# Kernel optimization log

Measured on AMD Instinct MI355X. Metric: run time of the kernel, lower is better.

Reference implementation:

```python
import jax, jax.numpy as jnp
import numpy as np

T, B, D = 200, 1024, 128
T_OBS = 140
L = 20       # rec_dims: encoder latent per mean/std
LAT = 32     # latents: generative latent dim
GRU_U = 200  # gru_units
UNITS = 100  # hidden units of ODE-func / z0 nets


def _lin(key, fan_in, fan_out):
    return jax.random.normal(key, (fan_in, fan_out), jnp.float32) / jnp.sqrt(jnp.float32(fan_in))


def setup_inputs() -> dict:
    key = jax.random.key(0)
    ks = jax.random.split(key, 20)
    gin = 2 * L + 2 * D  # GRU input: (mean,std) + (data,mask)
    inp = {
        "truth": jax.random.normal(ks[0], (T, B, D), jnp.float32),
        "t": jnp.arange(T, dtype=jnp.float32),
        "obs_idx": jnp.sort(jax.random.randint(ks[1], (T_OBS,), 0, T)),
        "eps": jax.random.normal(ks[2], (B, LAT), jnp.float32),
        # encoder ODE func (rec_layers=1 hidden layer of UNITS)
        "enc_w1": _lin(ks[3], L, UNITS), "enc_b1": jnp.zeros(UNITS, jnp.float32),
        "enc_w2": _lin(ks[4], UNITS, L), "enc_b2": jnp.zeros(L, jnp.float32),
        # GRU unit: update / reset / new-state nets
        "gru_uw1": _lin(ks[5], gin, GRU_U), "gru_ub1": jnp.zeros(GRU_U, jnp.float32),
        "gru_uw2": _lin(ks[6], GRU_U, 2 * L), "gru_ub2": jnp.zeros(2 * L, jnp.float32),
        "gru_rw1": _lin(ks[7], gin, GRU_U), "gru_rb1": jnp.zeros(GRU_U, jnp.float32),
        "gru_rw2": _lin(ks[8], GRU_U, 2 * L), "gru_rb2": jnp.zeros(2 * L, jnp.float32),
        "gru_nw1": _lin(ks[9], gin, GRU_U), "gru_nb1": jnp.zeros(GRU_U, jnp.float32),
        "gru_nw2": _lin(ks[10], GRU_U, 2 * L), "gru_nb2": jnp.zeros(2 * L, jnp.float32),
        # transform hidden -> z0 (mean,std)
        "z0_w1": _lin(ks[11], 2 * L, UNITS), "z0_b1": jnp.zeros(UNITS, jnp.float32),
        "z0_w2": _lin(ks[12], UNITS, 2 * LAT), "z0_b2": jnp.zeros(2 * LAT, jnp.float32),
        # decoder ODE func (gen_layers=2 hidden layers of UNITS)
        "dec_w1": _lin(ks[13], LAT, UNITS), "dec_b1": jnp.zeros(UNITS, jnp.float32),
        "dec_w2": _lin(ks[14], UNITS, UNITS), "dec_b2": jnp.zeros(UNITS, jnp.float32),
        "dec_w3": _lin(ks[15], UNITS, LAT), "dec_b3": jnp.zeros(LAT, jnp.float32),
        # readout latent -> data space
        "out_w": _lin(ks[16], LAT, D), "out_b": jnp.zeros(D, jnp.float32),
    }
    return inp


def _rk4(f, y, dt):
    k1 = f(y)
    k2 = f(y + 0.5 * dt * k1)
    k3 = f(y + 0.5 * dt * k2)
    k4 = f(y + dt * k3)
    return y + (dt / 6.0) * (k1 + 2.0 * k2 + 2.0 * k3 + k4)


def reference(truth, t, obs_idx, eps,
              enc_w1, enc_b1, enc_w2, enc_b2,
              gru_uw1, gru_ub1, gru_uw2, gru_ub2,
              gru_rw1, gru_rb1, gru_rw2, gru_rb2,
              gru_nw1, gru_nb1, gru_nw2, gru_nb2,
              z0_w1, z0_b1, z0_w2, z0_b2,
              dec_w1, dec_b1, dec_w2, dec_b2, dec_w3, dec_b3,
              out_w, out_b):
    enc_f = lambda y: jnp.tanh(y @ enc_w1 + enc_b1) @ enc_w2 + enc_b2
    dec_f = lambda z: (jnp.tanh(jnp.tanh(z @ dec_w1 + dec_b1) @ dec_w2 + dec_b2)
                       @ dec_w3 + dec_b3)

    # ----- ODE-RNN encoder, run_backwards=True over observed timesteps -----
    x_obs = truth[obs_idx][::-1]                     # [To, B, D], time-reversed
    t_obs = t[obs_idx][::-1]
    dts = jnp.concatenate([jnp.zeros(1, t.dtype), jnp.diff(t_obs)])  # <=0 steps

    def enc_step(carry, inp):
        ym, ys = carry                               # [B,L] each
        x, dt = inp
        ym = _rk4(enc_f, ym, dt)                     # evolve mean between obs
        xm = jnp.concatenate([x, jnp.ones_like(x)], -1)   # data + mask(=1)
        y = jnp.concatenate([ym, ys], -1)            # [B, 2L]
        yc = jnp.concatenate([y, xm], -1)            # [B, 2L+2D]
        u = jax.nn.sigmoid(jnp.tanh(yc @ gru_uw1 + gru_ub1) @ gru_uw2 + gru_ub2)
        r = jax.nn.sigmoid(jnp.tanh(yc @ gru_rw1 + gru_rb1) @ gru_rw2 + gru_rb2)
        nc = jnp.concatenate([y * r, xm], -1)
        ns = jnp.tanh(nc @ gru_nw1 + gru_nb1) @ gru_nw2 + gru_nb2
        nm, nsd = ns[:, :L], jnp.abs(ns[:, L:])
        new_y = (1.0 - u) * jnp.concatenate([nm, nsd], -1) + u * y
        return (new_y[:, :L], new_y[:, L:]), None

    nb = truth.shape[1]
    init = (jnp.zeros((nb, L), truth.dtype), jnp.zeros((nb, L), truth.dtype))
    (ym, ys), _ = jax.lax.scan(enc_step, init, (x_obs, dts))

    # ----- z0 posterior and sample (n_traj_samples=1) -----
    h = jnp.tanh(jnp.concatenate([ym, ys], -1) @ z0_w1 + z0_b1) @ z0_w2 + z0_b2
    z0_mean, z0_std = h[:, :LAT], jnp.abs(h[:, LAT:])
    z = z0_mean + eps * z0_std                       # [B, LAT]

    # ----- Neural ODE decoder over time_steps_to_predict = t -----
    def dec_step(zc, dt):
        zn = _rk4(dec_f, zc, dt)
        return zn, zn
    _, zs = jax.lax.scan(dec_step, z, jnp.diff(t))
    sol = jnp.concatenate([z[None], zs], 0)          # [T, B, LAT]

    out = sol @ out_w + out_b                        # [T, B, D]
    return jnp.transpose(out, (1, 0, 2))[None]       # [1, B, T, D]
```

## Files before the change

### kernel.cpp

```cpp
#include <hip/hip_runtime.h>
#include <math.h>

#define BB 1024
#define DD 128
#define NWG 256
#define CH 28
#define NCH 5

#define WS_WPACK 0
#define WS_B1E   81920
#define WS_W1Y   82560
#define WS_Y     106560
#define WS_Z     147520
#define WS_HPRE  180288
#define WS_SOL   180288

__device__ __forceinline__ float tanh_fast(float x) {
    const float t = __builtin_amdgcn_exp2f(x * 2.88539008177793f);
    return 1.f - 2.f * __builtin_amdgcn_rcpf(t + 1.f);
}

__global__ __launch_bounds__(256) void prep_kernel(
    const float* __restrict__ uw1, const float* __restrict__ ub1,
    const float* __restrict__ rw1, const float* __restrict__ rb1,
    const float* __restrict__ nw1, const float* __restrict__ nb1,
    float* __restrict__ ws)
{
    int tid = blockIdx.x * blockDim.x + threadIdx.x;
    int nth = gridDim.x * blockDim.x;
    for (int idx = tid; idx < 128 * 640; idx += nth) {
        int k = idx / 640, j = idx - k * 640;
        float v = 0.f;
        if (j < 600) {
            int g = j / 200, jj = j - g * 200;
            const float* w1 = (g == 0) ? uw1 : (g == 1) ? rw1 : nw1;
            v = w1[(40 + k) * 200 + jj];
        }
        ws[WS_WPACK + idx] = v;
    }
    for (int j = tid; j < 640; j += nth) {
        float s = 0.f;
        if (j < 600) {
            int g = j / 200, jj = j - g * 200;
            const float* w1 = (g == 0) ? uw1 : (g == 1) ? rw1 : nw1;
            const float* b1 = (g == 0) ? ub1 : (g == 1) ? rb1 : nb1;
            s = b1[jj];
            for (int k = 168; k < 296; ++k) s += w1[k * 200 + jj];
        }
        ws[WS_B1E + j] = s;
    }
    for (int idx = tid; idx < 40 * 600; idx += nth) {
        int k = idx / 600, j = idx - k * 600;
        int g = j / 200, jj = j - g * 200;
        const float* w1 = (g == 0) ? uw1 : (g == 1) ? rw1 : nw1;
        ws[WS_W1Y + idx] = w1[k * 200 + jj];
    }
}

__global__ __launch_bounds__(256) void hpre_gemm(
    const float* __restrict__ truth, const int* __restrict__ obs_idx,
    const float* __restrict__ ws, float* __restrict__ hpre, int s0)
{
    __shared__ float sx[64][68];
    __shared__ float sw[64][132];
    const int t0 = threadIdx.x;
    const int jt = blockIdx.x % 5;
    const int bt = (blockIdx.x / 5) % 16;
    const int sl = blockIdx.x / 80;
    const int oi = obs_idx[139 - (s0 + sl)];
    const int b0 = bt * 64;
    const float* wpack = ws + WS_WPACK;
    const float* b1e   = ws + WS_B1E;

    const int jj  = t0 & 15;
    const int bb4 = t0 >> 4;
    float acc[8][4];
#pragma unroll
    for (int m = 0; m < 8; ++m)
#pragma unroll
        for (int q = 0; q < 4; ++q) acc[m][q] = 0.f;

    for (int kh = 0; kh < 2; ++kh) {
        __syncthreads();
        for (int i = t0; i < 64 * 16; i += 256) {
            int bb = i >> 4, kq = i & 15;
            const float4 v = *(const float4*)&truth[((size_t)oi * BB + b0 + bb) * DD + kh * 64 + kq * 4];
            *(float4*)&sx[bb][kq * 4] = v;
        }
        for (int i = t0; i < 64 * 32; i += 256) {
            int kk = i >> 5, jq = i & 31;
            const float4 v = *(const float4*)&wpack[(kh * 64 + kk) * 640 + jt * 128 + jq * 4];
            *(float4*)&sw[kk][jq * 4] = v;
        }
        __syncthreads();
#pragma unroll 4
        for (int k = 0; k < 64; ++k) {
            float xv[4], wv[8];
#pragma unroll
            for (int q = 0; q < 4; ++q) xv[q] = sx[bb4 * 4 + q][k];
#pragma unroll
            for (int m = 0; m < 8; ++m) wv[m] = sw[k][jj + 16 * m];
#pragma unroll
            for (int m = 0; m < 8; ++m)
#pragma unroll
                for (int q = 0; q < 4; ++q) acc[m][q] += wv[m] * xv[q];
        }
    }
    const int bblk = bt * 16 + bb4;
#pragma unroll
    for (int m = 0; m < 8; ++m) {
        int j = jt * 128 + jj + 16 * m;
        if (j < 600) {
            float be = b1e[j];
#pragma unroll
            for (int q = 0; q < 4; ++q)
                hpre[(size_t)((sl * 256 + bblk) * 4 + q) * 600 + j] = acc[m][q] + be;
        }
    }
}

__global__ __launch_bounds__(256, 1) void enc_chunk(
    const float* __restrict__ tg, const int* __restrict__ obs_idx,
    const float* __restrict__ eps,
    const float* __restrict__ ew1, const float* __restrict__ eb1,
    const float* __restrict__ ew2, const float* __restrict__ eb2,
    const float* __restrict__ uw2, const float* __restrict__ ub2,
    const float* __restrict__ rw2, const float* __restrict__ rb2,
    const float* __restrict__ nw2, const float* __restrict__ nb2,
    const float* __restrict__ z0w1, const float* __restrict__ z0b1,
    const float* __restrict__ z0w2, const float* __restrict__ z0b2,
    float* __restrict__ ws, int s0)
{
    __shared__ float s_t[200];
    __shared__ int   s_oi[140];
    __shared__ __align__(16) float s_y[40][4];
    __shared__ __align__(16) float s_ytmp[20][4];
    __shared__ float s_kacc[20][4];
    __shared__ __align__(16) float s_hid[4][104];
    __shared__ float s_pe[20][4][2];
    __shared__ __align__(16) float s_ew1t[100 * 20];
    __shared__ __align__(16) float s_w2n[40 * 212];
    __shared__ __align__(16) float s_hur[4][416];
    __shared__ __align__(16) float s_hn[4][208];
    __shared__ float s_pw[80][4][4];
    __shared__ float s_pn[40][4][4];
    __shared__ float s_u[40][4];
    __shared__ __align__(16) float s_yr[40][4];
    __shared__ float s_z0o[4][64];

    const int t0 = threadIdx.x;
    const int bblk = blockIdx.x;
    const int b0 = bblk * 4;
    const float* hpre = ws + WS_HPRE;

    float rgy[3][40];
    float rew2h[52];
    float rw2q[2][52];
    float eb1_r = 0.f, eb2_r = 0.f, bur_r = 0.f, bn_r = 0.f;

    if (t0 < 200) {
#pragma unroll
        for (int g = 0; g < 3; ++g)
#pragma unroll
            for (int k = 0; k < 40; ++k)
                rgy[g][k] = ws[WS_W1Y + k * 600 + g * 200 + t0];
    }
    if (t0 < 100) eb1_r = eb1[t0];
    if (t0 < 160) {
        const int c2 = t0 % 20, kh = t0 / 80;
#pragma unroll
        for (int i = 0; i < 52; ++i) {
            const int row = kh * 52 + i;
            rew2h[i] = (row < 100) ? ew2[row * 20 + c2] : 0.f;
        }
    }
    if (t0 < 80) eb2_r = eb2[t0 % 20];
    if (t0 < 160) {
        const int p = t0 % 20, g = (t0 / 20) % 2, kq = t0 / 40;
        const float* w2 = g ? rw2 : uw2;
#pragma unroll
        for (int j = 0; j < 2; ++j)
#pragma unroll
            for (int i = 0; i < 52; ++i) {
                const int row = kq * 52 + i;
                rw2q[j][i] = (row < 200) ? w2[row * 40 + p + 20 * j] : 0.f;
            }
        bur_r = ((t0 % 80) < 40) ? ub2[t0 % 80] : rb2[(t0 % 80) - 40];
        bn_r = nb2[t0 % 40];
    }

    for (int i = t0; i < 2000; i += 256) { int k = i / 100, c = i % 100; s_ew1t[c * 20 + k] = ew1[i]; }
    for (int i = t0; i < 40 * 212; i += 256) { int o = i / 212, k = i % 212; s_w2n[i] = (k < 200) ? nw2[k * 40 + o] : 0.f; }
    for (int i = t0; i < 200; i += 256) s_t[i] = tg[i];
    for (int i = t0; i < 140; i += 256) s_oi[i] = obs_idx[i];
    if (t0 < 160) { int k = t0 % 40, b = t0 / 40; s_y[k][b] = s0 ? ws[WS_Y + k * 1024 + b0 + b] : 0.f; }
    if (t0 < 4) {
#pragma unroll
        for (int i = 0; i < 4; ++i) s_hid[t0][100 + i] = 0.f;
#pragma unroll
        for (int i = 0; i < 8; ++i) { s_hur[t0][200 + i] = 0.f; s_hur[t0][408 + i] = 0.f; s_hn[t0][200 + i] = 0.f; }
    }
    __syncthreads();

    for (int sl = 0; sl < CH; ++sl) {
        const int s = s0 + sl;
        const int oi = s_oi[139 - s];
        const float dt = (s == 0) ? 0.f : (s_t[oi] - s_t[s_oi[140 - s]]);

        float hpu[4], hpr[4], hpn[4];
        if (t0 < 200) {
#pragma unroll
            for (int q = 0; q < 4; ++q) {
                const size_t r = (size_t)((sl * 256 + bblk) * 4 + q) * 600;
                hpu[q] = hpre[r + t0];
                hpr[q] = hpre[r + 200 + t0];
                hpn[q] = hpre[r + 400 + t0];
            }
        }

#pragma unroll 1
        for (int e = 0; e < 4; ++e) {
            if (t0 < 100) {
                const int c = t0;
                float a[4] = {eb1_r, eb1_r, eb1_r, eb1_r};
#pragma unroll
                for (int i = 0; i < 5; ++i) {
                    const float4 wv = *(const float4*)&s_ew1t[c * 20 + 4 * i];
                    const float wk[4] = {wv.x, wv.y, wv.z, wv.w};
#pragma unroll
                    for (int kk = 0; kk < 4; ++kk) {
                        const int k = 4 * i + kk;
                        const float4 yv = (e == 0) ? *(const float4*)&s_y[k][0]
                                                   : *(const float4*)&s_ytmp[k][0];
                        a[0] += wk[kk] * yv.x; a[1] += wk[kk] * yv.y;
                        a[2] += wk[kk] * yv.z; a[3] += wk[kk] * yv.w;
                    }
                }
#pragma unroll
                for (int b = 0; b < 4; ++b) s_hid[b][c] = tanhf(a[b]);
            }
            __syncthreads();
            if (t0 < 160) {
                const int c2 = t0 % 20, b = (t0 / 20) % 4, kh = t0 / 80;
                float acc = 0.f;
#pragma unroll
                for (int i = 0; i < 13; ++i) {
                    const float4 hv = *(const float4*)&s_hid[b][kh * 52 + 4 * i];
                    acc += hv.x * rew2h[4 * i] + hv.y * rew2h[4 * i + 1]
                         + hv.z * rew2h[4 * i + 2] + hv.w * rew2h[4 * i + 3];
                }
                s_pe[c2][b][kh] = acc;
            }
            __syncthreads();
            if (t0 < 80) {
                const int c2 = t0 % 20, b = t0 / 20;
                const float kv = eb2_r + s_pe[c2][b][0] + s_pe[c2][b][1];
                const float y0 = s_y[c2][b];
                if (e == 0)      { s_kacc[c2][b] = kv;        s_ytmp[c2][b] = y0 + 0.5f * dt * kv; }
                else if (e == 1) { s_kacc[c2][b] += 2.f * kv; s_ytmp[c2][b] = y0 + 0.5f * dt * kv; }
                else if (e == 2) { s_kacc[c2][b] += 2.f * kv; s_ytmp[c2][b] = y0 + dt * kv; }
                else             { s_y[c2][b] = y0 + (dt / 6.f) * (s_kacc[c2][b] + kv); }
            }
            __syncthreads();
        }

        if (t0 < 200) {
            float au[4], ar[4];
#pragma unroll
            for (int b = 0; b < 4; ++b) { au[b] = hpu[b]; ar[b] = hpr[b]; }
#pragma unroll
            for (int k = 0; k < 40; ++k) {
                const float4 yv = *(const float4*)&s_y[k][0];
                const float wu = rgy[0][k], wr = rgy[1][k];
                au[0] += wu * yv.x; au[1] += wu * yv.y; au[2] += wu * yv.z; au[3] += wu * yv.w;
                ar[0] += wr * yv.x; ar[1] += wr * yv.y; ar[2] += wr * yv.z; ar[3] += wr * yv.w;
            }
#pragma unroll
            for (int b = 0; b < 4; ++b) {
                s_hur[b][t0] = tanhf(au[b]);
                s_hur[b][208 + t0] = tanhf(ar[b]);
            }
        }
        __syncthreads();

        if (t0 < 160) {
            const int p = t0 % 20, g = (t0 / 20) % 2, kq = t0 / 40;
            const int goff = g * 208;
            float a1[4] = {0.f, 0.f, 0.f, 0.f}, a2[4] = {0.f, 0.f, 0.f, 0.f};
#pragma unroll
            for (int i = 0; i < 13; ++i) {
                const float wa = rw2q[0][4 * i], wb = rw2q[0][4 * i + 1],
                            wc = rw2q[0][4 * i + 2], wd = rw2q[0][4 * i + 3];
                const float we = rw2q[1][4 * i], wf = rw2q[1][4 * i + 1],
                            wg = rw2q[1][4 * i + 2], wh = rw2q[1][4 * i + 3];
#pragma unroll
                for (int b = 0; b < 4; ++b) {
                    const float4 hv = *(const float4*)&s_hur[b][goff + kq * 52 + 4 * i];
                    a1[b] += hv.x * wa + hv.y * wb + hv.z * wc + hv.w * wd;
                    a2[b] += hv.x * we + hv.y * wf + hv.z * wg + hv.w * wh;
                }
            }
            const int o1 = 40 * g + p, o2 = o1 + 20;
#pragma unroll
            for (int b = 0; b < 4; ++b) { s_pw[o1][b][kq] = a1[b]; s_pw[o2][b][kq] = a2[b]; }
        }
        __syncthreads();

        if (t0 < 160) {
            const int o = t0 % 80, bp = t0 / 80;
#pragma unroll
            for (int j = 0; j < 2; ++j) {
                const int b = 2 * bp + j;
                const float v = bur_r + s_pw[o][b][0] + s_pw[o][b][1] + s_pw[o][b][2] + s_pw[o][b][3];
                const float sg = 1.f / (1.f + expf(-v));
                if (o < 40) s_u[o][b] = sg;
                else        s_yr[o - 40][b] = s_y[o - 40][b] * sg;
            }
        }
        __syncthreads();

        if (t0 < 200) {
            float an[4];
#pragma unroll
            for (int b = 0; b < 4; ++b) an[b] = hpn[b];
#pragma unroll
            for (int k = 0; k < 40; ++k) {
                const float4 yv = *(const float4*)&s_yr[k][0];
                const float w = rgy[2][k];
                an[0] += w * yv.x; an[1] += w * yv.y; an[2] += w * yv.z; an[3] += w * yv.w;
            }
#pragma unroll
            for (int b = 0; b < 4; ++b) s_hn[b][t0] = tanhf(an[b]);
        }
        __syncthreads();

        if (t0 < 160) {
            const int o = t0 % 40, kq = t0 / 40;
            float an[4] = {0.f, 0.f, 0.f, 0.f};
#pragma unroll
            for (int i = 0; i < 13; ++i) {
                const float4 wv = *(const float4*)&s_w2n[o * 212 + kq * 52 + 4 * i];
#pragma unroll
                for (int b = 0; b < 4; ++b) {
                    const float4 hv = *(const float4*)&s_hn[b][kq * 52 + 4 * i];
                    an[b] += hv.x * wv.x + hv.y * wv.y + hv.z * wv.z + hv.w * wv.w;
                }
            }
#pragma unroll
            for (int b = 0; b < 4; ++b) s_pn[o][b][kq] = an[b];
        }
        __syncthreads();

        if (t0 < 160) {
            const int o = t0 % 40, b = t0 / 40;
            const float v = bn_r + s_pn[o][b][0] + s_pn[o][b][1] + s_pn[o][b][2] + s_pn[o][b][3];
            const float cand = (o < 20) ? v : fabsf(v);
            const float uu = s_u[o][b];
            s_y[o][b] = (1.f - uu) * cand + uu * s_y[o][b];
        }
        __syncthreads();
    }

    if (s0 + CH == 140) {
        if (t0 < 100) {
            const int c = t0;
            float a[4] = {z0b1[c], z0b1[c], z0b1[c], z0b1[c]};
#pragma unroll
            for (int k = 0; k < 40; ++k) {
                const float4 yv = *(const float4*)&s_y[k][0];
                const float w = z0w1[k * 100 + c];
                a[0] += w * yv.x; a[1] += w * yv.y; a[2] += w * yv.z; a[3] += w * yv.w;
            }
#pragma unroll
            for (int b = 0; b < 4; ++b) s_hid[b][c] = tanhf(a[b]);
        }
        __syncthreads();
        {
            const int b = t0 / 64, u = t0 % 64;
            float acc = z0b2[u];
#pragma unroll
            for (int i = 0; i < 25; ++i) {
                const float4 hv = *(const float4*)&s_hid[b][4 * i];
                acc += hv.x * z0w2[(4 * i) * 64 + u] + hv.y * z0w2[(4 * i + 1) * 64 + u]
                     + hv.z * z0w2[(4 * i + 2) * 64 + u] + hv.w * z0w2[(4 * i + 3) * 64 + u];
            }
            s_z0o[b][u] = acc;
        }
        __syncthreads();
        if (t0 < 128) {
            const int b = t0 / 32, i = t0 % 32;
            const int gb = b0 + b;
            ws[WS_Z + gb * 32 + i] = s_z0o[b][i] + eps[gb * 32 + i] * fabsf(s_z0o[b][32 + i]);
        }
    }
    if (t0 < 160) {
        const int k = t0 % 40, b = t0 / 40;
        ws[WS_Y + k * 1024 + b0 + b] = s_y[k][b];
    }
}

__global__ __launch_bounds__(256, 3) void dec_kernel(
    const float* __restrict__ tg,
    const float* __restrict__ dw1, const float* __restrict__ db1,
    const float* __restrict__ dw2, const float* __restrict__ db2,
    const float* __restrict__ dw3, const float* __restrict__ db3,
    float* __restrict__ ws)
{
    __shared__ float s_t[200];
    __shared__ __align__(16) float s_z[32];
    __shared__ __align__(16) float s_h1[112];
    __shared__ __align__(16) float s_h2[112];
    __shared__ float s_p1[4][100];
    __shared__ float s_p2[4][100];
    __shared__ float s_p3[8][32];

    const int t0 = threadIdx.x;
    const int w  = t0 >> 6;
    const int l  = t0 & 63;
    const int hk = l >> 5;
    const int batch = blockIdx.x;

    const int c0 = l;
    const int c1 = 64 + l;
    const bool has1 = (l < 36);
    const int j3 = l & 31;

    float rw1a[8], rw1b[8], rw2a[28], rw2b[28], rw3[14];
#pragma unroll
    for (int i = 0; i < 8; ++i) {
        rw1a[i] = dw1[(8 * w + i) * 100 + c0];
        rw1b[i] = has1 ? dw1[(8 * w + i) * 100 + c1] : 0.f;
    }
#pragma unroll
    for (int i = 0; i < 28; ++i) {
        const int row = 28 * w + i;
        const bool v = (row < 100);
        rw2a[i] = v ? dw2[row * 100 + c0] : 0.f;
        rw2b[i] = (v && has1) ? dw2[row * 100 + c1] : 0.f;
    }
#pragma unroll
    for (int i = 0; i < 14; ++i) {
        const int row = 28 * w + 14 * hk + i;
        rw3[i] = (row < 100) ? dw3[row * 32 + j3] : 0.f;
    }
    float b1_r = 0.f, b2_r = 0.f, b3_r = 0.f;
    if (t0 < 100) { b1_r = db1[t0]; b2_r = db2[t0]; }
    if (t0 < 32)  b3_r = db3[t0];

    for (int i = t0; i < 200; i += 256) s_t[i] = tg[i];
    if (t0 >= 100 && t0 < 112) { s_h1[t0] = 0.f; s_h2[t0] = 0.f; }

    float z_r = 0.f, ka_r = 0.f;
    if (t0 < 32) { z_r = ws[WS_Z + (size_t)batch * 32 + t0]; s_z[t0] = z_r; }
    __syncthreads();

    for (int s = 0; s < 200; ++s) {
        if (t0 < 32)
            ws[WS_SOL + (size_t)(s * 1024 + batch) * 32 + t0] = z_r;
        if (s == 199) break;
        const float dtv = s_t[s + 1] - s_t[s];

#pragma unroll 1
        for (int e = 0; e < 4; ++e) {
            {
                const float4 za = *(const float4*)&s_z[8 * w];
                const float4 zb = *(const float4*)&s_z[8 * w + 4];
                float a0 = za.x * rw1a[0] + za.y * rw1a[1] + za.z * rw1a[2] + za.w * rw1a[3]
                         + zb.x * rw1a[4] + zb.y * rw1a[5] + zb.z * rw1a[6] + zb.w * rw1a[7];
                float a1 = za.x * rw1b[0] + za.y * rw1b[1] + za.z * rw1b[2] + za.w * rw1b[3]
                         + zb.x * rw1b[4] + zb.y * rw1b[5] + zb.z * rw1b[6] + zb.w * rw1b[7];
                s_p1[w][c0] = a0;
                if (has1) s_p1[w][c1] = a1;
            }
            __syncthreads();
            if (t0 < 100)
                s_h1[t0] = tanh_fast(b1_r + s_p1[0][t0] + s_p1[1][t0] + s_p1[2][t0] + s_p1[3][t0]);
            __syncthreads();

            {
                float a2 = 0.f, a3 = 0.f;
#pragma unroll
                for (int i = 0; i < 7; ++i) {
                    const float4 hv = *(const float4*)&s_h1[28 * w + 4 * i];
                    a2 += hv.x * rw2a[4 * i] + hv.y * rw2a[4 * i + 1]
                        + hv.z * rw2a[4 * i + 2] + hv.w * rw2a[4 * i + 3];
                    a3 += hv.x * rw2b[4 * i] + hv.y * rw2b[4 * i + 1]
                        + hv.z * rw2b[4 * i + 2] + hv.w * rw2b[4 * i + 3];
                }
                s_p2[w][c0] = a2;
                if (has1) s_p2[w][c1] = a3;
            }
            __syncthreads();
            if (t0 < 100)
                s_h2[t0] = tanh_fast(b2_r + s_p2[0][t0] + s_p2[1][t0] + s_p2[2][t0] + s_p2[3][t0]);
            __syncthreads();

            {
                float ap = 0.f;
#pragma unroll
                for (int i = 0; i < 7; ++i) {
                    const float2 hv = *(const float2*)&s_h2[28 * w + 14 * hk + 2 * i];
                    ap += hv.x * rw3[2 * i] + hv.y * rw3[2 * i + 1];
                }
                s_p3[2 * w + hk][j3] = ap;
            }
            __syncthreads();
            if (t0 < 32) {
                const float kj = b3_r
                    + s_p3[0][t0] + s_p3[1][t0] + s_p3[2][t0] + s_p3[3][t0]
                    + s_p3[4][t0] + s_p3[5][t0] + s_p3[6][t0] + s_p3[7][t0];
                float zs;
                if (e == 0)      { ka_r = kj;        zs = z_r + 0.5f * dtv * kj; }
                else if (e == 1) { ka_r += 2.f * kj; zs = z_r + 0.5f * dtv * kj; }
                else if (e == 2) { ka_r += 2.f * kj; zs = z_r + dtv * kj; }
                else             { z_r += (dtv / 6.f) * (ka_r + kj); zs = z_r; }
                s_z[t0] = zs;
            }
            __syncthreads();
        }
    }
}

__global__ __launch_bounds__(256) void proj_kernel(
    const float* __restrict__ ow, const float* __restrict__ ob,
    const float* __restrict__ ws, float* __restrict__ out)
{
    const int t0 = threadIdx.x;
    const int d = t0 & 127, half = t0 >> 7;
    float rw[32];
#pragma unroll
    for (int k = 0; k < 32; ++k) rw[k] = ow[k * 128 + d];
    const float bo = ob[d];
    const int sb0 = blockIdx.x * 64 + half * 32;
#pragma unroll 2
    for (int m = 0; m < 32; ++m) {
        const int sb = sb0 + m;
        const int s = sb >> 10, b = sb & 1023;
        const float4* zp = (const float4*)&ws[WS_SOL + (size_t)sb * 32];
        float acc = bo;
#pragma unroll
        for (int kq = 0; kq < 8; ++kq) {
            const float4 zv = zp[kq];
            acc += zv.x * rw[4 * kq] + zv.y * rw[4 * kq + 1]
                 + zv.z * rw[4 * kq + 2] + zv.w * rw[4 * kq + 3];
        }
        out[((size_t)b * 200 + s) * 128 + d] = acc;
    }
}

extern "C" void kernel_launch(void* const* d_in, const int* in_sizes, int n_in,
                              void* d_out, int out_size, void* d_ws, size_t ws_size,
                              hipStream_t stream)
{
    const float* truth = (const float*)d_in[0];
    const float* tg    = (const float*)d_in[1];
    const int*   oi    = (const int*)d_in[2];
    const float* eps   = (const float*)d_in[3];
    const float* ew1   = (const float*)d_in[4];
    const float* eb1   = (const float*)d_in[5];
    const float* ew2   = (const float*)d_in[6];
    const float* eb2   = (const float*)d_in[7];
    const float* uw1   = (const float*)d_in[8];
    const float* ub1   = (const float*)d_in[9];
    const float* uw2   = (const float*)d_in[10];
    const float* ub2   = (const float*)d_in[11];
    const float* rw1   = (const float*)d_in[12];
    const float* rb1   = (const float*)d_in[13];
    const float* rw2   = (const float*)d_in[14];
    const float* rb2   = (const float*)d_in[15];
    const float* nw1   = (const float*)d_in[16];
    const float* nb1   = (const float*)d_in[17];
    const float* nw2   = (const float*)d_in[18];
    const float* nb2   = (const float*)d_in[19];
    const float* z0w1  = (const float*)d_in[20];
    const float* z0b1  = (const float*)d_in[21];
    const float* z0w2  = (const float*)d_in[22];
    const float* z0b2  = (const float*)d_in[23];
    const float* dw1   = (const float*)d_in[24];
    const float* db1   = (const float*)d_in[25];
    const float* dw2   = (const float*)d_in[26];
    const float* db2   = (const float*)d_in[27];
    const float* dw3   = (const float*)d_in[28];
    const float* db3   = (const float*)d_in[29];
    const float* ow    = (const float*)d_in[30];
    const float* ob    = (const float*)d_in[31];
    float* ws  = (float*)d_ws;
    float* out = (float*)d_out;

    prep_kernel<<<dim3(120), dim3(256), 0, stream>>>(uw1, ub1, rw1, rb1, nw1, nb1, ws);
    for (int c = 0; c < NCH; ++c) {
        hpre_gemm<<<dim3(CH * 16 * 5), dim3(256), 0, stream>>>(truth, oi, ws, ws + WS_HPRE, c * CH);
        enc_chunk<<<dim3(NWG), dim3(256), 0, stream>>>(
            tg, oi, eps, ew1, eb1, ew2, eb2, uw2, ub2, rw2, rb2, nw2, nb2,
            z0w1, z0b1, z0w2, z0b2, ws, c * CH);
    }
    dec_kernel<<<dim3(1024), dim3(256), 0, stream>>>(tg, dw1, db1, dw2, db2, dw3, db3, ws);
    proj_kernel<<<dim3(3200), dim3(256), 0, stream>>>(ow, ob, ws, out);
}
```

Before: 4.514 ms.

## Cut decoder RK4 barriers by having each wave reduce its own hidden rows

The decoder ODE loop is re-partitioned so each wave owns a contiguous slice of hidden rows (24 or 28). That wave reduces the partial sums for its rows, applies tanh and consumes only those rows in the next layer. Every wave also redundantly computes the final k and z update for all 32 latents. Together these remove three of the six block-wide barriers per RK4 function evaluation, which matters in this latency-bound single-batch-per-block loop. In exchange the partial-sum buffers are padded and the last-layer matmul does more per-wave work with redundant reductions. Correctness now relies on intra-wave LDS ordering and on the benign race of waves writing identical s_z values.

```diff
diff --git a/kernel.cpp b/kernel.cpp
--- a/kernel.cpp
+++ b/kernel.cpp
@@ -408,24 +408,25 @@
 {
     __shared__ float s_t[200];
     __shared__ __align__(16) float s_z[32];
-    __shared__ __align__(16) float s_h1[112];
-    __shared__ __align__(16) float s_h2[112];
-    __shared__ float s_p1[4][100];
-    __shared__ float s_p2[4][100];
-    __shared__ float s_p3[8][32];
+    __shared__ __align__(16) float s_h1[100];
+    __shared__ __align__(16) float s_h2[100];
+    __shared__ float s_p1[4][128];
+    __shared__ float s_p2[4][128];
+    __shared__ float s_p3[4][32];
 
     const int t0 = threadIdx.x;
     const int w  = t0 >> 6;
     const int l  = t0 & 63;
-    const int hk = l >> 5;
     const int batch = blockIdx.x;
 
     const int c0 = l;
     const int c1 = 64 + l;
     const bool has1 = (l < 36);
     const int j3 = l & 31;
-
-    float rw1a[8], rw1b[8], rw2a[28], rw2b[28], rw3[14];
+    const int r0 = 24 * w;
+    const int n2 = (w == 3) ? 28 : 24;
+
+    float rw1a[8], rw1b[8], rw2a[28], rw2b[28], rw3[28];
 #pragma unroll
     for (int i = 0; i < 8; ++i) {
         rw1a[i] = dw1[(8 * w + i) * 100 + c0];
@@ -433,25 +434,21 @@
     }
 #pragma unroll
     for (int i = 0; i < 28; ++i) {
-        const int row = 28 * w + i;
-        const bool v = (row < 100);
+        const int row = r0 + i;
+        const bool v = (i < n2);
         rw2a[i] = v ? dw2[row * 100 + c0] : 0.f;
         rw2b[i] = (v && has1) ? dw2[row * 100 + c1] : 0.f;
-    }
-#pragma unroll
-    for (int i = 0; i < 14; ++i) {
-        const int row = 28 * w + 14 * hk + i;
-        rw3[i] = (row < 100) ? dw3[row * 32 + j3] : 0.f;
-    }
-    float b1_r = 0.f, b2_r = 0.f, b3_r = 0.f;
-    if (t0 < 100) { b1_r = db1[t0]; b2_r = db2[t0]; }
-    if (t0 < 32)  b3_r = db3[t0];
+        rw3[i]  = v ? dw3[row * 32 + j3] : 0.f;
+    }
+    float b1c = 0.f, b2c = 0.f;
+    if (l < n2) { b1c = db1[r0 + l]; b2c = db2[r0 + l]; }
+    const float b3c = db3[j3];
 
     for (int i = t0; i < 200; i += 256) s_t[i] = tg[i];
-    if (t0 >= 100 && t0 < 112) { s_h1[t0] = 0.f; s_h2[t0] = 0.f; }
-
-    float z_r = 0.f, ka_r = 0.f;
-    if (t0 < 32) { z_r = ws[WS_Z + (size_t)batch * 32 + t0]; s_z[t0] = z_r; }
+
+    float z_r = ws[WS_Z + (size_t)batch * 32 + j3];
+    float ka_r = 0.f;
+    if (l < 32) s_z[l] = z_r;
     __syncthreads();
 
     for (int s = 0; s < 200; ++s) {
@@ -470,53 +467,76 @@
                 float a1 = za.x * rw1b[0] + za.y * rw1b[1] + za.z * rw1b[2] + za.w * rw1b[3]
                          + zb.x * rw1b[4] + zb.y * rw1b[5] + zb.z * rw1b[6] + zb.w * rw1b[7];
                 s_p1[w][c0] = a0;
-                if (has1) s_p1[w][c1] = a1;
+                s_p1[w][c1] = a1;
             }
             __syncthreads();
-            if (t0 < 100)
-                s_h1[t0] = tanh_fast(b1_r + s_p1[0][t0] + s_p1[1][t0] + s_p1[2][t0] + s_p1[3][t0]);
-            __syncthreads();
+
+            if (l < n2) {
+                const int r = r0 + l;
+                s_h1[r] = tanh_fast(b1c + s_p1[0][r] + s_p1[1][r] + s_p1[2][r] + s_p1[3][r]);
+            }
 
             {
                 float a2 = 0.f, a3 = 0.f;
-#pragma unroll
-                for (int i = 0; i < 7; ++i) {
-                    const float4 hv = *(const float4*)&s_h1[28 * w + 4 * i];
-                    a2 += hv.x * rw2a[4 * i] + hv.y * rw2a[4 * i + 1]
-                        + hv.z * rw2a[4 * i + 2] + hv.w * rw2a[4 * i + 3];
-                    a3 += hv.x * rw2b[4 * i] + hv.y * rw2b[4 * i + 1]
-                        + hv.z * rw2b[4 * i + 2] + hv.w * rw2b[4 * i + 3];
+                if (w == 3) {
+#pragma unroll
+                    for (int i = 0; i < 7; ++i) {
+                        const float4 hv = *(const float4*)&s_h1[72 + 4 * i];
+                        a2 += hv.x * rw2a[4 * i] + hv.y * rw2a[4 * i + 1]
+                            + hv.z * rw2a[4 * i + 2] + hv.w * rw2a[4 * i + 3];
+                        a3 += hv.x * rw2b[4 * i] + hv.y * rw2b[4 * i + 1]
+                            + hv.z * rw2b[4 * i + 2] + hv.w * rw2b[4 * i + 3];
+                    }
+                } else {
+#pragma unroll
+                    for (int i = 0; i < 6; ++i) {
+                        const float4 hv = *(const float4*)&s_h1[r0 + 4 * i];
+                        a2 += hv.x * rw2a[4 * i] + hv.y * rw2a[4 * i + 1]
+                            + hv.z * rw2a[4 * i + 2] + hv.w * rw2a[4 * i + 3];
+                        a3 += hv.x * rw2b[4 * i] + hv.y * rw2b[4 * i + 1]
+                            + hv.z * rw2b[4 * i + 2] + hv.w * rw2b[4 * i + 3];
+                    }
                 }
                 s_p2[w][c0] = a2;
-                if (has1) s_p2[w][c1] = a3;
+                s_p2[w][c1] = a3;
             }
             __syncthreads();
-            if (t0 < 100)
-                s_h2[t0] = tanh_fast(b2_r + s_p2[0][t0] + s_p2[1][t0] + s_p2[2][t0] + s_p2[3][t0]);
-            __syncthreads();
+
+            if (l < n2) {
+                const int r = r0 + l;
+                s_h2[r] = tanh_fast(b2c + s_p2[0][r] + s_p2[1][r] + s_p2[2][r] + s_p2[3][r]);
+            }
 
             {
                 float ap = 0.f;
-#pragma unroll
-                for (int i = 0; i < 7; ++i) {
-                    const float2 hv = *(const float2*)&s_h2[28 * w + 14 * hk + 2 * i];
-                    ap += hv.x * rw3[2 * i] + hv.y * rw3[2 * i + 1];
+                if (w == 3) {
+#pragma unroll
+                    for (int i = 0; i < 7; ++i) {
+                        const float4 hv = *(const float4*)&s_h2[72 + 4 * i];
+                        ap += hv.x * rw3[4 * i] + hv.y * rw3[4 * i + 1]
+                            + hv.z * rw3[4 * i + 2] + hv.w * rw3[4 * i + 3];
+                    }
+                } else {
+#pragma unroll
+                    for (int i = 0; i < 6; ++i) {
+                        const float4 hv = *(const float4*)&s_h2[r0 + 4 * i];
+                        ap += hv.x * rw3[4 * i] + hv.y * rw3[4 * i + 1]
+                            + hv.z * rw3[4 * i + 2] + hv.w * rw3[4 * i + 3];
+                    }
                 }
-                s_p3[2 * w + hk][j3] = ap;
+                if (l < 32) s_p3[w][l] = ap;
             }
             __syncthreads();
-            if (t0 < 32) {
-                const float kj = b3_r
-                    + s_p3[0][t0] + s_p3[1][t0] + s_p3[2][t0] + s_p3[3][t0]
-                    + s_p3[4][t0] + s_p3[5][t0] + s_p3[6][t0] + s_p3[7][t0];
+
+            {
+                const float kj = b3c + s_p3[0][j3] + s_p3[1][j3] + s_p3[2][j3] + s_p3[3][j3];
                 float zs;
                 if (e == 0)      { ka_r = kj;        zs = z_r + 0.5f * dtv * kj; }
                 else if (e == 1) { ka_r += 2.f * kj; zs = z_r + 0.5f * dtv * kj; }
                 else if (e == 2) { ka_r += 2.f * kj; zs = z_r + dtv * kj; }
                 else             { z_r += (dtv / 6.f) * (ka_r + kj); zs = z_r; }
-                s_z[t0] = zs;
-            }
-            __syncthreads();
+                if (l < 32) s_z[l] = zs;
+            }
         }
     }
 }
```

Result: slower. 4.700 ms (+4.1%).
